# Kernel tuning notes

Measured on AMD Instinct MI355X. Metric: run time of the kernel, lower is better.

## Reference

```python
import jax, jax.numpy as jnp
import numpy as np

POOL = 14
NUM_ROIS = 512
H, W, C = 200, 200, 1024


def setup_inputs() -> dict:
    key = jax.random.key(0)
    k1, k2, k3, k4, k5 = jax.random.split(key, 5)
    img = jax.random.normal(k1, (1, H, W, C), dtype=jnp.float32)
    # valid boxes: x + w <= W, y + h <= H, w,h >= 8
    x = jax.random.randint(k2, (1, NUM_ROIS), 0, W // 2)
    y = jax.random.randint(k3, (1, NUM_ROIS), 0, H // 2)
    w = jax.random.randint(k4, (1, NUM_ROIS), 8, W // 2)
    h = jax.random.randint(k5, (1, NUM_ROIS), 8, H // 2)
    rois = jnp.stack([x, y, w, h], axis=-1).astype(jnp.int32)  # [1, R, 4]
    return {"img": img, "rois": rois}


def _roi_resize(fm, box):
    # fm: [H, W, C]; box: [4] int32 (x, y, w, h)
    x, y, w, h = box[0], box[1], box[2], box[3]
    # TF1 tf.image.resize_images bilinear, align_corners=False (asymmetric):
    # src = dst * (in_size / out_size), taps floored + clamped to crop extent.
    sy = jnp.arange(POOL, dtype=jnp.float32) * (h.astype(jnp.float32) / POOL)
    sx = jnp.arange(POOL, dtype=jnp.float32) * (w.astype(jnp.float32) / POOL)
    y0 = jnp.floor(sy).astype(jnp.int32)
    x0 = jnp.floor(sx).astype(jnp.int32)
    y0c = jnp.clip(y0, 0, h - 1)
    y1c = jnp.clip(y0 + 1, 0, h - 1)
    x0c = jnp.clip(x0, 0, w - 1)
    x1c = jnp.clip(x0 + 1, 0, w - 1)
    wy = (sy - y0.astype(jnp.float32))[:, None, None]  # [P,1,1]
    wx = (sx - x0.astype(jnp.float32))[None, :, None]  # [1,P,1]
    iy0, iy1 = y + y0c, y + y1c  # absolute row indices
    ix0, ix1 = x + x0c, x + x1c  # absolute col indices
    g00 = fm[iy0[:, None], ix0[None, :]]  # [P,P,C]
    g01 = fm[iy0[:, None], ix1[None, :]]
    g10 = fm[iy1[:, None], ix0[None, :]]
    g11 = fm[iy1[:, None], ix1[None, :]]
    top = g00 + (g01 - g00) * wx
    bot = g10 + (g11 - g10) * wx
    return top + (bot - top) * wy


def reference(img, rois):
    fm = img[0]  # [H, W, C]
    out = jax.vmap(lambda b: _roi_resize(fm, b))(rois[0])  # [R, P, P, C]
    return out[None]  # [1, R, P, P, C]
```

## Files before the change

### kernel.cpp

```cpp
#include <hip/hip_runtime.h>

#define POOL 14
#define NUM_ROIS 512
#define IMG_H 200
#define IMG_W 200
#define IMG_C 1024
#define NUM_XCD 8

typedef float v4f __attribute__((ext_vector_type(4)));

__global__ __launch_bounds__(256) void roi_row_kernel(
    const float* __restrict__ img,
    const int*   __restrict__ rois,
    float*       __restrict__ out)
{
    const int b   = blockIdx.x;
    const int xcd = b & (NUM_XCD - 1);
    const int s   = b >> 3;
    const int roi_in = s / POOL;
    const int py     = s - roi_in * POOL;
    const int r      = xcd * (NUM_ROIS / NUM_XCD) + roi_in;

    const int4 box = ((const int4*)rois)[r];
    const int bx = box.x, by = box.y, bw = box.z, bh = box.w;

    const float stepy = (float)bh / (float)POOL;
    const float stepx = (float)bw / (float)POOL;

    const float sy = (float)py * stepy;
    const int   y0 = (int)floorf(sy);
    const float wy = sy - (float)y0;
    const int y0c = min(max(y0, 0), bh - 1);
    const int y1c = min(max(y0 + 1, 0), bh - 1);

    const float* __restrict__ row0 = img + (size_t)(by + y0c) * IMG_W * IMG_C;
    const float* __restrict__ row1 = img + (size_t)(by + y1c) * IMG_W * IMG_C;

    const int c = threadIdx.x * 4;
    float* __restrict__ orow =
        out + ((size_t)r * (POOL * POOL) + (size_t)py * POOL) * IMG_C + c;

#pragma unroll
    for (int px = 0; px < POOL; ++px) {
        const float sx = (float)px * stepx;
        const int   x0 = (int)floorf(sx);
        const float wx = sx - (float)x0;
        const int x0c = min(max(x0, 0), bw - 1);
        const int x1c = min(max(x0 + 1, 0), bw - 1);
        const int ix0 = bx + x0c;
        const int ix1 = bx + x1c;

        const v4f g00 = *(const v4f*)(row0 + (size_t)ix0 * IMG_C + c);
        const v4f g01 = *(const v4f*)(row0 + (size_t)ix1 * IMG_C + c);
        const v4f g10 = *(const v4f*)(row1 + (size_t)ix0 * IMG_C + c);
        const v4f g11 = *(const v4f*)(row1 + (size_t)ix1 * IMG_C + c);

        const v4f top = g00 + (g01 - g00) * wx;
        const v4f bot = g10 + (g11 - g10) * wx;
        const v4f res = top + (bot - top) * wy;

        __builtin_nontemporal_store(res, (v4f*)(orow + (size_t)px * IMG_C));
    }
}

extern "C" void kernel_launch(void* const* d_in, const int* in_sizes, int n_in,
                              void* d_out, int out_size, void* d_ws, size_t ws_size,
                              hipStream_t stream) {
    const float* img  = (const float*)d_in[0];
    const int*   rois = (const int*)d_in[1];
    float*       out  = (float*)d_out;

    const int num_blocks = NUM_ROIS * POOL;
    roi_row_kernel<<<num_blocks, 256, 0, stream>>>(img, rois, out);
}
```

Measured before the change: 627.9 us.

## Reorder ROI row work items by source row per XCD via counting-sort kernel

```diff
diff --git a/kernel.cpp b/kernel.cpp
--- a/kernel.cpp
+++ b/kernel.cpp
@@ -6,20 +6,96 @@
 #define IMG_W 200
 #define IMG_C 1024
 #define NUM_XCD 8
+#define ROIS_PER_XCD (NUM_ROIS / NUM_XCD)
+#define ITEMS_PER_XCD (ROIS_PER_XCD * POOL)
+#define XBINS 8
+#define NBINS (IMG_H * XBINS)
+#define BINS_PER_THREAD 7
 
 typedef float v4f __attribute__((ext_vector_type(4)));
+
+__device__ __forceinline__ int item_key(const int* __restrict__ rois,
+                                        int xcd, int i, int* out_code) {
+    const int roi_in = i / POOL;
+    const int py     = i - roi_in * POOL;
+    const int r      = xcd * ROIS_PER_XCD + roi_in;
+    const int4 box   = ((const int4*)rois)[r];
+    const float stepy = (float)box.w / (float)POOL;
+    const float sy    = (float)py * stepy;
+    const int y0  = (int)floorf(sy);
+    const int y0c = min(max(y0, 0), box.w - 1);
+    const int row = box.y + y0c;
+    *out_code = (r << 4) | py;
+    return row * XBINS + (box.x >> 5);
+}
+
+__global__ __launch_bounds__(256) void order_kernel(
+    const int* __restrict__ rois, int* __restrict__ perm) {
+    const int xcd = blockIdx.x;
+    const int tid = threadIdx.x;
+    __shared__ int hist[NBINS];
+    __shared__ int cnt[NBINS];
+    __shared__ int partial[256];
+
+    for (int k = tid; k < NBINS; k += 256) { hist[k] = 0; cnt[k] = 0; }
+    __syncthreads();
+
+    for (int i = tid; i < ITEMS_PER_XCD; i += 256) {
+        int code;
+        atomicAdd(&hist[item_key(rois, xcd, i, &code)], 1);
+    }
+    __syncthreads();
+
+    const int b0 = tid * BINS_PER_THREAD;
+    int lsum[BINS_PER_THREAD];
+    int local = 0;
+    for (int j = 0; j < BINS_PER_THREAD; ++j) {
+        const int k = b0 + j;
+        lsum[j] = local;
+        if (k < NBINS) local += hist[k];
+    }
+    partial[tid] = local;
+    __syncthreads();
+    for (int off = 1; off < 256; off <<= 1) {
+        const int add = (tid >= off) ? partial[tid - off] : 0;
+        __syncthreads();
+        partial[tid] += add;
+        __syncthreads();
+    }
+    const int chunk_excl = partial[tid] - local;
+    for (int j = 0; j < BINS_PER_THREAD; ++j) {
+        const int k = b0 + j;
+        if (k < NBINS) hist[k] = chunk_excl + lsum[j];
+    }
+    __syncthreads();
+
+    for (int i = tid; i < ITEMS_PER_XCD; i += 256) {
+        int code;
+        const int key = item_key(rois, xcd, i, &code);
+        const int pos = hist[key] + atomicAdd(&cnt[key], 1);
+        perm[xcd * ITEMS_PER_XCD + pos] = code;
+    }
+}
 
 __global__ __launch_bounds__(256) void roi_row_kernel(
     const float* __restrict__ img,
     const int*   __restrict__ rois,
+    const int*   __restrict__ perm,
     float*       __restrict__ out)
 {
-    const int b   = blockIdx.x;
-    const int xcd = b & (NUM_XCD - 1);
-    const int s   = b >> 3;
-    const int roi_in = s / POOL;
-    const int py     = s - roi_in * POOL;
-    const int r      = xcd * (NUM_ROIS / NUM_XCD) + roi_in;
+    const int b = blockIdx.x;
+    int r, py;
+    if (perm) {
+        const int code = perm[(b & (NUM_XCD - 1)) * ITEMS_PER_XCD + (b >> 3)];
+        r  = code >> 4;
+        py = code & 15;
+    } else {
+        const int xcd = b & (NUM_XCD - 1);
+        const int s   = b >> 3;
+        const int roi_in = s / POOL;
+        py = s - roi_in * POOL;
+        r  = xcd * ROIS_PER_XCD + roi_in;
+    }
 
     const int4 box = ((const int4*)rois)[r];
     const int bx = box.x, by = box.y, bw = box.z, bh = box.w;
@@ -70,6 +146,10 @@
     const int*   rois = (const int*)d_in[1];
     float*       out  = (float*)d_out;
 
-    const int num_blocks = NUM_ROIS * POOL;
-    roi_row_kernel<<<num_blocks, 256, 0, stream>>>(img, rois, out);
+    int* perm = nullptr;
+    if (d_ws && ws_size >= (size_t)(NUM_XCD * ITEMS_PER_XCD) * sizeof(int)) {
+        perm = (int*)d_ws;
+        order_kernel<<<NUM_XCD, 256, 0, stream>>>(rois, perm);
+    }
+    roi_row_kernel<<<NUM_ROIS * POOL, 256, 0, stream>>>(img, rois, perm, out);
 }
```

Result: faster. 576.5 us (-8.2%).
